# Performance work log

Hardware: AMD Instinct MI355X
Metric: run time of the kernel (lower is better)

## Reference

```python
import jax, jax.numpy as jnp
import numpy as np

N_NODES = 50000
N_EDGES = 800000
IN_FEAT = 4
HIDDEN = 128
NUM_LAYERS = 3


def setup_inputs() -> dict:
    key = jax.random.key(0)
    ks = jax.random.split(key, 16)
    x = jax.random.normal(ks[0], (N_NODES, IN_FEAT), dtype=jnp.float32)
    edge_index = jax.random.randint(ks[1], (2, N_EDGES), 0, N_NODES, dtype=jnp.int64)

    def lin(k, fan_in, fan_out):
        bound = 1.0 / np.sqrt(fan_in)
        k1, k2 = jax.random.split(k)
        W = jax.random.uniform(k1, (fan_in, fan_out), minval=-bound, maxval=bound, dtype=jnp.float32)
        b = jax.random.uniform(k2, (fan_out,), minval=-bound, maxval=bound, dtype=jnp.float32)
        return W, b

    W_enc, b_enc = lin(ks[2], IN_FEAT, HIDDEN)
    W_g1, b_g1 = lin(ks[3], HIDDEN, HIDDEN)
    W_g2, b_g2 = lin(ks[4], HIDDEN, HIDDEN)
    W_g3, b_g3 = lin(ks[5], HIDDEN, HIDDEN)
    W_m1, b_m1 = lin(ks[6], 2 * HIDDEN, HIDDEN)
    W_m2, b_m2 = lin(ks[7], HIDDEN, 3)
    return {
        "x": x, "edge_index": edge_index,
        "W_enc": W_enc, "b_enc": b_enc,
        "W_g1": W_g1, "b_g1": b_g1,
        "W_g2": W_g2, "b_g2": b_g2,
        "W_g3": W_g3, "b_g3": b_g3,
        "W_m1": W_m1, "b_m1": b_m1,
        "W_m2": W_m2, "b_m2": b_m2,
    }


def _gcn_forward(x, edge_index, W_enc, b_enc, gcn_params, W_m1, b_m1, W_m2, b_m2):
    n = x.shape[0]
    # Node encoder (linear + ReLU) -> [N, H]
    h = jax.nn.relu(x @ W_enc + b_enc)

    # Add self-loops once (GCNConv default add_self_loops=True)
    src = jnp.concatenate([edge_index[0], jnp.arange(n, dtype=edge_index.dtype)])
    dst = jnp.concatenate([edge_index[1], jnp.arange(n, dtype=edge_index.dtype)])
    # Symmetric degree normalization: D^{-1/2} (A+I) D^{-1/2}
    deg = jax.ops.segment_sum(jnp.ones_like(dst, dtype=h.dtype), dst, num_segments=n)
    deg_inv_sqrt = jnp.where(deg > 0, jax.lax.rsqrt(jnp.maximum(deg, 1.0)), 0.0)
    norm = (deg_inv_sqrt[src] * deg_inv_sqrt[dst])[:, None]  # [E+N, 1]

    for (W, b) in gcn_params:
        m = (h @ W)[src] * norm                       # gather + scale messages
        h = jax.ops.segment_sum(m, dst, num_segments=n) + b
        h = jax.nn.relu(h)                            # dropout is identity at eval

    # Edge classifier: gather endpoints, concat, MLP -> [E, 3]
    ef = jnp.concatenate([h[edge_index[0]], h[edge_index[1]]], axis=-1)
    return jax.nn.relu(ef @ W_m1 + b_m1) @ W_m2 + b_m2


def reference(x, edge_index, W_enc, b_enc, W_g1, b_g1, W_g2, b_g2, W_g3, b_g3, W_m1, b_m1, W_m2, b_m2):
    gcn_params = [(W_g1, b_g1), (W_g2, b_g2), (W_g3, b_g3)]
    return _gcn_forward(x, edge_index, W_enc, b_enc, gcn_params, W_m1, b_m1, W_m2, b_m2)
```

## Files before the change

kernel.cpp:

```cpp
#include <hip/hip_runtime.h>
#include <hip/hip_bf16.h>

#define N_NODES 50000
#define N_EDGES 800000
#define HID 128
#define NBUCKET 1024
#define N_NODE_BLOCKS ((N_NODES + 255) / 256)

typedef __attribute__((ext_vector_type(8))) short bf16x8;
typedef __attribute__((ext_vector_type(4))) float f32x4;

__device__ __forceinline__ ushort f2bf(float f) {
    uint u = __float_as_uint(f);
    return (ushort)((u + 0x7FFFu + ((u >> 16) & 1u)) >> 16);
}
__device__ __forceinline__ float bf2f(ushort h) { return __uint_as_float(((uint)h) << 16); }

__global__ void k_count(const int* __restrict__ ei, int* cnt) {
    int e = blockIdx.x * blockDim.x + threadIdx.x;
    if (e < N_EDGES) atomicAdd(&cnt[ei[N_EDGES + e]], 1);
}

__global__ __launch_bounds__(256) void k_bhist(const int* __restrict__ cnt, int* gHist,
                                               int* __restrict__ blockBase) {
    __shared__ int lh[NBUCKET];
    int t = threadIdx.x;
    for (int d = t; d < NBUCKET; d += 256) lh[d] = 0;
    __syncthreads();
    int n = blockIdx.x * 256 + t;
    if (n < N_NODES) {
        int deg = min(cnt[n], NBUCKET - 1);
        atomicAdd(&lh[deg], 1);
    }
    __syncthreads();
    for (int d = t; d < NBUCKET; d += 256) {
        int c = lh[d];
        blockBase[blockIdx.x * NBUCKET + d] = c ? atomicAdd(&gHist[d], c) : 0;
    }
}

__global__ __launch_bounds__(NBUCKET) void k_prefix(const int* __restrict__ gHist,
                                                    int* __restrict__ histBase,
                                                    int* __restrict__ edgeBase,
                                                    int* __restrict__ rowStartP) {
    __shared__ int a[NBUCKET];
    __shared__ int b[NBUCKET];
    int t = threadIdx.x;
    int h = gHist[t];
    a[t] = h;
    b[t] = h * t;
    __syncthreads();
    for (int off = 1; off < NBUCKET; off <<= 1) {
        int av = (t >= off) ? a[t - off] : 0;
        int bv = (t >= off) ? b[t - off] : 0;
        __syncthreads();
        a[t] += av;
        b[t] += bv;
        __syncthreads();
    }
    histBase[t] = a[t] - h;
    edgeBase[t] = b[t] - h * t;
    if (t == 0) rowStartP[N_NODES] = N_EDGES;
}

__global__ __launch_bounds__(256) void k_rank(const int* __restrict__ cnt,
                                              const int* __restrict__ histBase,
                                              const int* __restrict__ edgeBase,
                                              const int* __restrict__ blockBase,
                                              int* __restrict__ rank,
                                              int* __restrict__ rowStartP,
                                              float* __restrict__ dinvP) {
    __shared__ int cur[NBUCKET];
    int t = threadIdx.x;
    for (int d = t; d < NBUCKET; d += 256) cur[d] = 0;
    __syncthreads();
    int n = blockIdx.x * 256 + t;
    if (n < N_NODES) {
        int deg = min(cnt[n], NBUCKET - 1);
        int slot = atomicAdd(&cur[deg], 1);
        int r = histBase[deg] + blockBase[blockIdx.x * NBUCKET + deg] + slot;
        rank[n] = r;
        rowStartP[r] = edgeBase[deg] + (r - histBase[deg]) * deg;
        dinvP[r] = rsqrtf(1.0f + (float)deg);
    }
}

__global__ void k_fill(const int* __restrict__ ei, const int* __restrict__ rank,
                       const int* __restrict__ rowStartP, int* cursorP,
                       int2* __restrict__ csrE) {
    int e = blockIdx.x * blockDim.x + threadIdx.x;
    if (e < N_EDGES) {
        int s = ei[e];
        int d = ei[N_EDGES + e];
        int rd = rank[d];
        int pos = rowStartP[rd] + atomicAdd(&cursorP[rd], 1);
        csrE[pos] = make_int2(rank[s], e);
    }
}

struct WSplitArgs {
    const float* src[5];
    ushort* th[5];
    ushort* tl[5];
};

__global__ void k_tsplit5(WSplitArgs a) {
    int i = blockIdx.x * 256 + threadIdx.x;
    int which = i >> 14, r = i & 16383;
    int k = r >> 7, j = r & 127;
    float v = a.src[which][r];
    ushort hi = f2bf(v);
    a.th[which][j * 128 + k] = hi;
    a.tl[which][j * 128 + k] = f2bf(v - bf2f(hi));
}

__global__ void k_encoder(const float* __restrict__ x, const float* __restrict__ W,
                          const float* __restrict__ b, const int* __restrict__ rank,
                          ushort* __restrict__ hH, ushort* __restrict__ hL) {
    int i = blockIdx.x * 256 + threadIdx.x;
    int n = i >> 6, l = i & 63;
    int j = l * 2;
    float4 xv = *(const float4*)(x + (size_t)n * 4);
    float2 acc = *(const float2*)(b + j);
    float2 w0 = *(const float2*)(W + 0 * 128 + j);
    float2 w1 = *(const float2*)(W + 1 * 128 + j);
    float2 w2 = *(const float2*)(W + 2 * 128 + j);
    float2 w3 = *(const float2*)(W + 3 * 128 + j);
    acc.x += xv.x * w0.x + xv.y * w1.x + xv.z * w2.x + xv.w * w3.x;
    acc.y += xv.x * w0.y + xv.y * w1.y + xv.z * w2.y + xv.w * w3.y;
    float v0 = fmaxf(acc.x, 0.f), v1 = fmaxf(acc.y, 0.f);
    ushort h0 = f2bf(v0), h1 = f2bf(v1);
    ushort l0 = f2bf(v0 - bf2f(h0)), l1 = f2bf(v1 - bf2f(h1));
    size_t o = (size_t)rank[n] * 64 + l;
    ((uint*)hH)[o] = (uint)h0 | ((uint)h1 << 16);
    ((uint*)hL)[o] = (uint)l0 | ((uint)l1 << 16);
}

__global__ __launch_bounds__(256) void k_gemm_mfma(const ushort* __restrict__ AH,
                                                   const ushort* __restrict__ AL,
                                                   const ushort* __restrict__ BTH,
                                                   const ushort* __restrict__ BTL,
                                                   float* __restrict__ out,
                                                   const float* __restrict__ scale, int M) {
    int tid = threadIdx.x;
    int w = tid >> 6, l = tid & 63;
    int ln = l & 15, lk = l >> 4;
    int r0 = blockIdx.x * 128 + w * 32;
    int row0 = r0 + ln, row1 = r0 + 16 + ln;
    int a0 = row0 < M ? row0 : M - 1;
    int a1 = row1 < M ? row1 : M - 1;

    f32x4 acc0[8] = {};
    f32x4 acc1[8] = {};
#pragma unroll
    for (int kc = 0; kc < 4; ++kc) {
        int ko = kc * 32 + lk * 8;
        bf16x8 h0H = *(const bf16x8*)(AH + (size_t)a0 * 128 + ko);
        bf16x8 h0L = *(const bf16x8*)(AL + (size_t)a0 * 128 + ko);
        bf16x8 h1H = *(const bf16x8*)(AH + (size_t)a1 * 128 + ko);
        bf16x8 h1L = *(const bf16x8*)(AL + (size_t)a1 * 128 + ko);
#pragma unroll
        for (int nt = 0; nt < 8; ++nt) {
            size_t boff = (size_t)(nt * 16 + ln) * 128 + ko;
            bf16x8 wH = *(const bf16x8*)(BTH + boff);
            bf16x8 wL = *(const bf16x8*)(BTL + boff);
            acc0[nt] = __builtin_amdgcn_mfma_f32_16x16x32_bf16(wH, h0H, acc0[nt], 0, 0, 0);
            acc0[nt] = __builtin_amdgcn_mfma_f32_16x16x32_bf16(wL, h0H, acc0[nt], 0, 0, 0);
            acc0[nt] = __builtin_amdgcn_mfma_f32_16x16x32_bf16(wH, h0L, acc0[nt], 0, 0, 0);
            acc1[nt] = __builtin_amdgcn_mfma_f32_16x16x32_bf16(wH, h1H, acc1[nt], 0, 0, 0);
            acc1[nt] = __builtin_amdgcn_mfma_f32_16x16x32_bf16(wL, h1H, acc1[nt], 0, 0, 0);
            acc1[nt] = __builtin_amdgcn_mfma_f32_16x16x32_bf16(wH, h1L, acc1[nt], 0, 0, 0);
        }
    }
    float s0v = scale[a0];
    float s1v = scale[a1];
#pragma unroll
    for (int nt = 0; nt < 8; ++nt) {
        int jb = nt * 16 + lk * 4;
        if (row0 < M) {
            *(float4*)(out + (size_t)row0 * 128 + jb) =
                make_float4(acc0[nt][0] * s0v, acc0[nt][1] * s0v, acc0[nt][2] * s0v, acc0[nt][3] * s0v);
        }
        if (row1 < M) {
            *(float4*)(out + (size_t)row1 * 128 + jb) =
                make_float4(acc1[nt][0] * s1v, acc1[nt][1] * s1v, acc1[nt][2] * s1v, acc1[nt][3] * s1v);
        }
    }
}

__global__ __launch_bounds__(1024, 2) void k_agg_gemm(
    const float* __restrict__ hw, const float* __restrict__ bg,
    const float* __restrict__ dinvP, const int* __restrict__ rowStartP,
    const int2* __restrict__ csrE,
    const ushort* __restrict__ BTH1, const ushort* __restrict__ BTL1,
    const ushort* __restrict__ BTH2, const ushort* __restrict__ BTL2,
    float* __restrict__ out1, float* __restrict__ out2,
    const float* __restrict__ b1, const float* __restrict__ outScale) {
    __shared__ uint AsH[16][68];
    __shared__ uint AsL[16][68];
    int tid = threadIdx.x;
    int w = tid >> 6, l = tid & 63;
    int g = l >> 4, li = l & 15;
    int c8 = li * 8;
    int n = blockIdx.x * 16 + w;

    float4 aA, aB;
    if (g == 0) {
        aA = *(const float4*)(hw + (size_t)n * 128 + c8);
        aB = *(const float4*)(hw + (size_t)n * 128 + c8 + 4);
    } else {
        aA = make_float4(0.f, 0.f, 0.f, 0.f);
        aB = aA;
    }
    int s0 = rowStartP[n], s1 = rowStartP[n + 1];
    int k = s0 + g;
    float4 v0a = make_float4(0.f, 0.f, 0.f, 0.f), v0b = v0a;
    if (k < s1) {
        const float* r = hw + (size_t)csrE[k].x * 128 + c8;
        v0a = *(const float4*)(r);
        v0b = *(const float4*)(r + 4);
    }
    for (; k < s1; k += 4) {
        float4 v1a = make_float4(0.f, 0.f, 0.f, 0.f), v1b = v1a;
        if (k + 4 < s1) {
            const float* r = hw + (size_t)csrE[k + 4].x * 128 + c8;
            v1a = *(const float4*)(r);
            v1b = *(const float4*)(r + 4);
        }
        aA.x += v0a.x; aA.y += v0a.y; aA.z += v0a.z; aA.w += v0a.w;
        aB.x += v0b.x; aB.y += v0b.y; aB.z += v0b.z; aB.w += v0b.w;
        v0a = v1a;
        v0b = v1b;
    }
    aA.x += __shfl_xor(aA.x, 16); aA.y += __shfl_xor(aA.y, 16);
    aA.z += __shfl_xor(aA.z, 16); aA.w += __shfl_xor(aA.w, 16);
    aB.x += __shfl_xor(aB.x, 16); aB.y += __shfl_xor(aB.y, 16);
    aB.z += __shfl_xor(aB.z, 16); aB.w += __shfl_xor(aB.w, 16);
    aA.x += __shfl_xor(aA.x, 32); aA.y += __shfl_xor(aA.y, 32);
    aA.z += __shfl_xor(aA.z, 32); aA.w += __shfl_xor(aA.w, 32);
    aB.x += __shfl_xor(aB.x, 32); aB.y += __shfl_xor(aB.y, 32);
    aB.z += __shfl_xor(aB.z, 32); aB.w += __shfl_xor(aB.w, 32);

    if (g == 0) {
        float di = dinvP[n];
        float4 bbA = *(const float4*)(bg + c8);
        float4 bbB = *(const float4*)(bg + c8 + 4);
        float f0 = fmaxf(bbA.x + di * aA.x, 0.f);
        float f1 = fmaxf(bbA.y + di * aA.y, 0.f);
        float f2 = fmaxf(bbA.z + di * aA.z, 0.f);
        float f3 = fmaxf(bbA.w + di * aA.w, 0.f);
        float f4 = fmaxf(bbB.x + di * aB.x, 0.f);
        float f5 = fmaxf(bbB.y + di * aB.y, 0.f);
        float f6 = fmaxf(bbB.z + di * aB.z, 0.f);
        float f7 = fmaxf(bbB.w + di * aB.w, 0.f);
        ushort h0 = f2bf(f0), h1 = f2bf(f1), h2 = f2bf(f2), h3 = f2bf(f3);
        ushort h4 = f2bf(f4), h5 = f2bf(f5), h6 = f2bf(f6), h7 = f2bf(f7);
        uint4 uh = make_uint4((uint)h0 | ((uint)h1 << 16), (uint)h2 | ((uint)h3 << 16),
                              (uint)h4 | ((uint)h5 << 16), (uint)h6 | ((uint)h7 << 16));
        ushort l0 = f2bf(f0 - bf2f(h0)), l1 = f2bf(f1 - bf2f(h1));
        ushort l2 = f2bf(f2 - bf2f(h2)), l3 = f2bf(f3 - bf2f(h3));
        ushort l4 = f2bf(f4 - bf2f(h4)), l5 = f2bf(f5 - bf2f(h5));
        ushort l6 = f2bf(f6 - bf2f(h6)), l7 = f2bf(f7 - bf2f(h7));
        uint4 ul = make_uint4((uint)l0 | ((uint)l1 << 16), (uint)l2 | ((uint)l3 << 16),
                              (uint)l4 | ((uint)l5 << 16), (uint)l6 | ((uint)l7 << 16));
        *(uint4*)&AsH[w][li * 4] = uh;
        *(uint4*)&AsL[w][li * 4] = ul;
    }
    __syncthreads();

    bool second = w >= 8;
    if (second && !BTH2) return;
    const ushort* TH = second ? BTH2 : BTH1;
    const ushort* TL = second ? BTL2 : BTL1;
    int ln = l & 15, lk = l >> 4;
    int ct = w & 7;
    int node = blockIdx.x * 16 + ln;
    f32x4 acc = {};
#pragma unroll
    for (int kc = 0; kc < 4; ++kc) {
        uint4 uh = *(uint4*)&AsH[ln][kc * 16 + lk * 4];
        uint4 ul = *(uint4*)&AsL[ln][kc * 16 + lk * 4];
        bf16x8 hh, hl;
        __builtin_memcpy(&hh, &uh, 16);
        __builtin_memcpy(&hl, &ul, 16);
        size_t boff = (size_t)(ct * 16 + ln) * 128 + kc * 32 + lk * 8;
        bf16x8 wh = *(const bf16x8*)(TH + boff);
        bf16x8 wl = *(const bf16x8*)(TL + boff);
        acc = __builtin_amdgcn_mfma_f32_16x16x32_bf16(wh, hh, acc, 0, 0, 0);
        acc = __builtin_amdgcn_mfma_f32_16x16x32_bf16(wl, hh, acc, 0, 0, 0);
        acc = __builtin_amdgcn_mfma_f32_16x16x32_bf16(wh, hl, acc, 0, 0, 0);
    }
    int jb = ct * 16 + lk * 4;
    if (outScale) {
        float s = outScale[node];
        *(float4*)(out1 + (size_t)node * 128 + jb) =
            make_float4(acc[0] * s, acc[1] * s, acc[2] * s, acc[3] * s);
    } else if (!second) {
        *(float4*)(out1 + (size_t)node * 128 + jb) =
            make_float4(acc[0], acc[1], acc[2], acc[3]);
    } else {
        float4 bv = *(const float4*)(b1 + jb);
        *(float4*)(out2 + (size_t)node * 128 + jb) =
            make_float4(acc[0] + bv.x, acc[1] + bv.y, acc[2] + bv.z, acc[3] + bv.w);
    }
}

__global__ __launch_bounds__(256) void k_edge_final(const float* __restrict__ P,
                                                    const float* __restrict__ Qb,
                                                    const int* __restrict__ rowStartP,
                                                    const int2* __restrict__ csrE,
                                                    const float* __restrict__ W2,
                                                    const float* __restrict__ b2,
                                                    float* __restrict__ out) {
    int wid = (blockIdx.x * 256 + threadIdx.x) >> 6;
    int l = threadIdx.x & 63;
    if (wid >= N_NODES) return;
    int s0 = rowStartP[wid], s1 = rowStartP[wid + 1];
    if (s0 >= s1) return;
    int j8 = (l & 15) * 8;
    int g = l >> 4;

    float4 qa = *(const float4*)(Qb + (size_t)wid * 128 + j8);
    float4 qb = *(const float4*)(Qb + (size_t)wid * 128 + j8 + 4);
    float w2r[8][3];
#pragma unroll
    for (int k = 0; k < 8; ++k) {
        w2r[k][0] = W2[(j8 + k) * 3 + 0];
        w2r[k][1] = W2[(j8 + k) * 3 + 1];
        w2r[k][2] = W2[(j8 + k) * 3 + 2];
    }
    float bz0 = b2[0], bz1 = b2[1], bz2 = b2[2];

    int k = s0 + g;
    int2 c = make_int2(0, 0);
    float4 pa = make_float4(0.f, 0.f, 0.f, 0.f), pb = pa;
    if (k < s1) {
        c = csrE[k];
        const float* pr = P + (size_t)c.x * 128 + j8;
        pa = *(const float4*)(pr);
        pb = *(const float4*)(pr + 4);
    }
    for (; k < s1; k += 4) {
        int kn = k + 4;
        int2 cn = make_int2(0, 0);
        float4 pan = make_float4(0.f, 0.f, 0.f, 0.f), pbn = pan;
        if (kn < s1) {
            cn = csrE[kn];
            const float* prn = P + (size_t)cn.x * 128 + j8;
            pan = *(const float4*)(prn);
            pbn = *(const float4*)(prn + 4);
        }
        float z[8];
        z[0] = fmaxf(pa.x + qa.x, 0.f);
        z[1] = fmaxf(pa.y + qa.y, 0.f);
        z[2] = fmaxf(pa.z + qa.z, 0.f);
        z[3] = fmaxf(pa.w + qa.w, 0.f);
        z[4] = fmaxf(pb.x + qb.x, 0.f);
        z[5] = fmaxf(pb.y + qb.y, 0.f);
        z[6] = fmaxf(pb.z + qb.z, 0.f);
        z[7] = fmaxf(pb.w + qb.w, 0.f);
        float o0 = 0.f, o1 = 0.f, o2 = 0.f;
#pragma unroll
        for (int q = 0; q < 8; ++q) {
            o0 += z[q] * w2r[q][0];
            o1 += z[q] * w2r[q][1];
            o2 += z[q] * w2r[q][2];
        }
#pragma unroll
        for (int m = 1; m < 16; m <<= 1) {
            o0 += __shfl_xor(o0, m);
            o1 += __shfl_xor(o1, m);
            o2 += __shfl_xor(o2, m);
        }
        if ((l & 15) == 0) {
            float* op = out + (size_t)c.y * 3;
            op[0] = o0 + bz0;
            op[1] = o1 + bz1;
            op[2] = o2 + bz2;
        }
        c = cn;
        pa = pan;
        pb = pbn;
    }
}

extern "C" void kernel_launch(void* const* d_in, const int* in_sizes, int n_in,
                              void* d_out, int out_size, void* d_ws, size_t ws_size,
                              hipStream_t stream) {
    const float* x     = (const float*)d_in[0];
    const int*   ei    = (const int*)d_in[1];
    const float* W_enc = (const float*)d_in[2];
    const float* b_enc = (const float*)d_in[3];
    const float* Wg[3] = {(const float*)d_in[4], (const float*)d_in[6], (const float*)d_in[8]};
    const float* bg[3] = {(const float*)d_in[5], (const float*)d_in[7], (const float*)d_in[9]};
    const float* W_m1  = (const float*)d_in[10];
    const float* b_m1  = (const float*)d_in[11];
    const float* W_m2  = (const float*)d_in[12];
    const float* b_m2  = (const float*)d_in[13];
    float* out = (float*)d_out;

    char* w = (char*)d_ws;
    ushort* hH      = (ushort*)w;  w += (size_t)N_NODES * HID * 2;
    ushort* hL      = (ushort*)w;  w += (size_t)N_NODES * HID * 2;
    float*  bufA    = (float*)w;   w += (size_t)N_NODES * HID * 4;
    float*  bufB    = (float*)w;   w += (size_t)N_NODES * HID * 4;
    int2*   csrE    = (int2*)w;    w += (size_t)N_EDGES * 8;
    int*    cnt     = (int*)w;     w += (size_t)N_NODES * 4;
    int*    cursorP = (int*)w;     w += (size_t)N_NODES * 4;
    int*    gHist   = (int*)w;     w += NBUCKET * 4;
    size_t  zeroBytes = (size_t)(N_NODES * 2 + NBUCKET) * 4;
    int*    rank    = (int*)w;     w += (size_t)N_NODES * 4;
    int*    rowStartP = (int*)w;   w += (size_t)(N_NODES + 4) * 4;
    float*  dinvP   = (float*)w;   w += (size_t)N_NODES * 4;
    int*    histBase = (int*)w;    w += NBUCKET * 4;
    int*    edgeBase = (int*)w;    w += NBUCKET * 4;
    int*    blockBase = (int*)w;   w += (size_t)N_NODE_BLOCKS * NBUCKET * 4;
    ushort* WgTH[3], *WgTL[3];
    for (int i = 0; i < 3; ++i) {
        WgTH[i] = (ushort*)w; w += 128 * 128 * 2;
        WgTL[i] = (ushort*)w; w += 128 * 128 * 2;
    }
    ushort* WtTH = (ushort*)w; w += 128 * 128 * 2;
    ushort* WtTL = (ushort*)w; w += 128 * 128 * 2;
    ushort* WbTH = (ushort*)w; w += 128 * 128 * 2;
    ushort* WbTL = (ushort*)w; w += 128 * 128 * 2;

    float* P  = (float*)hH;
    float* Qb = bufB;

    hipMemsetAsync(cnt, 0, zeroBytes, stream);
    k_count<<<(N_EDGES + 255) / 256, 256, 0, stream>>>(ei, cnt);
    k_bhist<<<N_NODE_BLOCKS, 256, 0, stream>>>(cnt, gHist, blockBase);
    k_prefix<<<1, NBUCKET, 0, stream>>>(gHist, histBase, edgeBase, rowStartP);
    k_rank<<<N_NODE_BLOCKS, 256, 0, stream>>>(cnt, histBase, edgeBase, blockBase,
                                              rank, rowStartP, dinvP);
    k_fill<<<(N_EDGES + 255) / 256, 256, 0, stream>>>(ei, rank, rowStartP, cursorP, csrE);

    WSplitArgs wa;
    wa.src[0] = Wg[0]; wa.th[0] = WgTH[0]; wa.tl[0] = WgTL[0];
    wa.src[1] = Wg[1]; wa.th[1] = WgTH[1]; wa.tl[1] = WgTL[1];
    wa.src[2] = Wg[2]; wa.th[2] = WgTH[2]; wa.tl[2] = WgTL[2];
    wa.src[3] = W_m1;             wa.th[3] = WtTH; wa.tl[3] = WtTL;
    wa.src[4] = W_m1 + 128 * 128; wa.th[4] = WbTH; wa.tl[4] = WbTL;
    k_tsplit5<<<5 * 16384 / 256, 256, 0, stream>>>(wa);

    k_encoder<<<N_NODES * 64 / 256, 256, 0, stream>>>(x, W_enc, b_enc, rank, hH, hL);

    k_gemm_mfma<<<(N_NODES + 127) / 128, 256, 0, stream>>>(hH, hL, WgTH[0], WgTL[0],
                                                           bufA, dinvP, N_NODES);

    const int fusedGrid = N_NODES / 16;
    k_agg_gemm<<<fusedGrid, 1024, 0, stream>>>(bufA, bg[0], dinvP, rowStartP, csrE,
                                               WgTH[1], WgTL[1], nullptr, nullptr,
                                               bufB, nullptr, nullptr, dinvP);
    k_agg_gemm<<<fusedGrid, 1024, 0, stream>>>(bufB, bg[1], dinvP, rowStartP, csrE,
                                               WgTH[2], WgTL[2], nullptr, nullptr,
                                               bufA, nullptr, nullptr, dinvP);
    k_agg_gemm<<<fusedGrid, 1024, 0, stream>>>(bufA, bg[2], dinvP, rowStartP, csrE,
                                               WtTH, WtTL, WbTH, WbTL,
                                               P, Qb, b_m1, nullptr);

    k_edge_final<<<(N_NODES * 64) / 256, 256, 0, stream>>>(P, Qb, rowStartP, csrE,
                                                           W_m2, b_m2, out);
}
```

Baseline: 467.4 us.

## Split fused aggregate+GEMM into separate kernels and fuse encoder into first GEMM

The old 1024-thread kernel fused aggregation with a small 16-row MFMA GEMM per block. It is replaced by a standalone aggregation kernel that writes bf16 hi/lo features, followed by the larger 128-row tiled MFMA GEMM. The final P/Q projection now runs in one launch with a 2D grid. The encoder is fused into the first GEMM, using an inverse rank map so inputs are gathered directly into shared memory. This trades extra global round-trips of the hidden features for better GEMM weight reuse and aggregation occupancy.

```diff
diff --git a/kernel.cpp b/kernel.cpp
--- a/kernel.cpp
+++ b/kernel.cpp
@@ -68,6 +68,7 @@
                                               const int* __restrict__ edgeBase,
                                               const int* __restrict__ blockBase,
                                               int* __restrict__ rank,
+                                              int* __restrict__ invRank,
                                               int* __restrict__ rowStartP,
                                               float* __restrict__ dinvP) {
     __shared__ int cur[NBUCKET];
@@ -80,6 +81,7 @@
         int slot = atomicAdd(&cur[deg], 1);
         int r = histBase[deg] + blockBase[blockIdx.x * NBUCKET + deg] + slot;
         rank[n] = r;
+        invRank[r] = n;
         rowStartP[r] = edgeBase[deg] + (r - histBase[deg]) * deg;
         dinvP[r] = rsqrtf(1.0f + (float)deg);
     }
@@ -114,105 +116,94 @@
     a.tl[which][j * 128 + k] = f2bf(v - bf2f(hi));
 }
 
-__global__ void k_encoder(const float* __restrict__ x, const float* __restrict__ W,
-                          const float* __restrict__ b, const int* __restrict__ rank,
-                          ushort* __restrict__ hH, ushort* __restrict__ hL) {
-    int i = blockIdx.x * 256 + threadIdx.x;
-    int n = i >> 6, l = i & 63;
-    int j = l * 2;
-    float4 xv = *(const float4*)(x + (size_t)n * 4);
-    float2 acc = *(const float2*)(b + j);
-    float2 w0 = *(const float2*)(W + 0 * 128 + j);
-    float2 w1 = *(const float2*)(W + 1 * 128 + j);
-    float2 w2 = *(const float2*)(W + 2 * 128 + j);
-    float2 w3 = *(const float2*)(W + 3 * 128 + j);
-    acc.x += xv.x * w0.x + xv.y * w1.x + xv.z * w2.x + xv.w * w3.x;
-    acc.y += xv.x * w0.y + xv.y * w1.y + xv.z * w2.y + xv.w * w3.y;
-    float v0 = fmaxf(acc.x, 0.f), v1 = fmaxf(acc.y, 0.f);
-    ushort h0 = f2bf(v0), h1 = f2bf(v1);
-    ushort l0 = f2bf(v0 - bf2f(h0)), l1 = f2bf(v1 - bf2f(h1));
-    size_t o = (size_t)rank[n] * 64 + l;
-    ((uint*)hH)[o] = (uint)h0 | ((uint)h1 << 16);
-    ((uint*)hL)[o] = (uint)l0 | ((uint)l1 << 16);
-}
-
-__global__ __launch_bounds__(256) void k_gemm_mfma(const ushort* __restrict__ AH,
-                                                   const ushort* __restrict__ AL,
-                                                   const ushort* __restrict__ BTH,
-                                                   const ushort* __restrict__ BTL,
-                                                   float* __restrict__ out,
-                                                   const float* __restrict__ scale, int M) {
-    int tid = threadIdx.x;
-    int w = tid >> 6, l = tid & 63;
-    int ln = l & 15, lk = l >> 4;
-    int r0 = blockIdx.x * 128 + w * 32;
-    int row0 = r0 + ln, row1 = r0 + 16 + ln;
-    int a0 = row0 < M ? row0 : M - 1;
-    int a1 = row1 < M ? row1 : M - 1;
-
-    f32x4 acc0[8] = {};
-    f32x4 acc1[8] = {};
-#pragma unroll
-    for (int kc = 0; kc < 4; ++kc) {
-        int ko = kc * 32 + lk * 8;
-        bf16x8 h0H = *(const bf16x8*)(AH + (size_t)a0 * 128 + ko);
-        bf16x8 h0L = *(const bf16x8*)(AL + (size_t)a0 * 128 + ko);
-        bf16x8 h1H = *(const bf16x8*)(AH + (size_t)a1 * 128 + ko);
-        bf16x8 h1L = *(const bf16x8*)(AL + (size_t)a1 * 128 + ko);
-#pragma unroll
-        for (int nt = 0; nt < 8; ++nt) {
-            size_t boff = (size_t)(nt * 16 + ln) * 128 + ko;
-            bf16x8 wH = *(const bf16x8*)(BTH + boff);
-            bf16x8 wL = *(const bf16x8*)(BTL + boff);
-            acc0[nt] = __builtin_amdgcn_mfma_f32_16x16x32_bf16(wH, h0H, acc0[nt], 0, 0, 0);
-            acc0[nt] = __builtin_amdgcn_mfma_f32_16x16x32_bf16(wL, h0H, acc0[nt], 0, 0, 0);
-            acc0[nt] = __builtin_amdgcn_mfma_f32_16x16x32_bf16(wH, h0L, acc0[nt], 0, 0, 0);
-            acc1[nt] = __builtin_amdgcn_mfma_f32_16x16x32_bf16(wH, h1H, acc1[nt], 0, 0, 0);
-            acc1[nt] = __builtin_amdgcn_mfma_f32_16x16x32_bf16(wL, h1H, acc1[nt], 0, 0, 0);
-            acc1[nt] = __builtin_amdgcn_mfma_f32_16x16x32_bf16(wH, h1L, acc1[nt], 0, 0, 0);
-        }
-    }
-    float s0v = scale[a0];
-    float s1v = scale[a1];
-#pragma unroll
-    for (int nt = 0; nt < 8; ++nt) {
-        int jb = nt * 16 + lk * 4;
-        if (row0 < M) {
-            *(float4*)(out + (size_t)row0 * 128 + jb) =
-                make_float4(acc0[nt][0] * s0v, acc0[nt][1] * s0v, acc0[nt][2] * s0v, acc0[nt][3] * s0v);
-        }
-        if (row1 < M) {
-            *(float4*)(out + (size_t)row1 * 128 + jb) =
-                make_float4(acc1[nt][0] * s1v, acc1[nt][1] * s1v, acc1[nt][2] * s1v, acc1[nt][3] * s1v);
-        }
-    }
-}
-
-__global__ __launch_bounds__(1024, 2) void k_agg_gemm(
-    const float* __restrict__ hw, const float* __restrict__ bg,
-    const float* __restrict__ dinvP, const int* __restrict__ rowStartP,
-    const int2* __restrict__ csrE,
-    const ushort* __restrict__ BTH1, const ushort* __restrict__ BTL1,
-    const ushort* __restrict__ BTH2, const ushort* __restrict__ BTL2,
-    float* __restrict__ out1, float* __restrict__ out2,
-    const float* __restrict__ b1, const float* __restrict__ outScale) {
+__global__ __launch_bounds__(512, 8) void k_enc_gemm(
+    const float* __restrict__ x, const float* __restrict__ Wenc,
+    const float* __restrict__ benc, const int* __restrict__ invRank,
+    const float* __restrict__ dinvP,
+    const ushort* __restrict__ BTH, const ushort* __restrict__ BTL,
+    float* __restrict__ out) {
     __shared__ uint AsH[16][68];
     __shared__ uint AsL[16][68];
     int tid = threadIdx.x;
+
+    if (tid < 256) {
+        int ln = tid >> 4, li = tid & 15;
+        int r = blockIdx.x * 16 + ln;
+        int n = invRank[r];
+        float4 xv = *(const float4*)(x + (size_t)n * 4);
+        int j0 = li * 8;
+        uint uh[4], ul[4];
+#pragma unroll
+        for (int p = 0; p < 4; ++p) {
+            ushort hs[2], ls[2];
+#pragma unroll
+            for (int q = 0; q < 2; ++q) {
+                int j = j0 + p * 2 + q;
+                float acc = benc[j];
+                acc += xv.x * Wenc[0 * 128 + j];
+                acc += xv.y * Wenc[1 * 128 + j];
+                acc += xv.z * Wenc[2 * 128 + j];
+                acc += xv.w * Wenc[3 * 128 + j];
+                float v = fmaxf(acc, 0.f);
+                hs[q] = f2bf(v);
+                ls[q] = f2bf(v - bf2f(hs[q]));
+            }
+            uh[p] = (uint)hs[0] | ((uint)hs[1] << 16);
+            ul[p] = (uint)ls[0] | ((uint)ls[1] << 16);
+        }
+        *(uint4*)&AsH[ln][li * 4] = make_uint4(uh[0], uh[1], uh[2], uh[3]);
+        *(uint4*)&AsL[ln][li * 4] = make_uint4(ul[0], ul[1], ul[2], ul[3]);
+    }
+    __syncthreads();
+
     int w = tid >> 6, l = tid & 63;
+    int ln = l & 15, lk = l >> 4;
+    int ct = w;
+    int node = blockIdx.x * 16 + ln;
+    f32x4 acc = {};
+#pragma unroll
+    for (int kc = 0; kc < 4; ++kc) {
+        uint4 uhv = *(uint4*)&AsH[ln][kc * 16 + lk * 4];
+        uint4 ulv = *(uint4*)&AsL[ln][kc * 16 + lk * 4];
+        bf16x8 hh, hl;
+        __builtin_memcpy(&hh, &uhv, 16);
+        __builtin_memcpy(&hl, &ulv, 16);
+        size_t boff = (size_t)(ct * 16 + ln) * 128 + kc * 32 + lk * 8;
+        bf16x8 wh = *(const bf16x8*)(BTH + boff);
+        bf16x8 wl = *(const bf16x8*)(BTL + boff);
+        acc = __builtin_amdgcn_mfma_f32_16x16x32_bf16(wh, hh, acc, 0, 0, 0);
+        acc = __builtin_amdgcn_mfma_f32_16x16x32_bf16(wl, hh, acc, 0, 0, 0);
+        acc = __builtin_amdgcn_mfma_f32_16x16x32_bf16(wh, hl, acc, 0, 0, 0);
+    }
+    int jb = ct * 16 + lk * 4;
+    float s = dinvP[node];
+    *(float4*)(out + (size_t)node * 128 + jb) =
+        make_float4(acc[0] * s, acc[1] * s, acc[2] * s, acc[3] * s);
+}
+
+__global__ __launch_bounds__(256) void k_aggregate(const float* __restrict__ hw,
+                                                   const float* __restrict__ bg,
+                                                   const float* __restrict__ dinvP,
+                                                   const int* __restrict__ rowStartP,
+                                                   const int2* __restrict__ csrE,
+                                                   ushort* __restrict__ hH,
+                                                   ushort* __restrict__ hL) {
+    int wid = (blockIdx.x * 256 + threadIdx.x) >> 6;
+    int l = threadIdx.x & 63;
+    if (wid >= N_NODES) return;
     int g = l >> 4, li = l & 15;
     int c8 = li * 8;
-    int n = blockIdx.x * 16 + w;
 
     float4 aA, aB;
     if (g == 0) {
-        aA = *(const float4*)(hw + (size_t)n * 128 + c8);
-        aB = *(const float4*)(hw + (size_t)n * 128 + c8 + 4);
+        aA = *(const float4*)(hw + (size_t)wid * 128 + c8);
+        aB = *(const float4*)(hw + (size_t)wid * 128 + c8 + 4);
     } else {
         aA = make_float4(0.f, 0.f, 0.f, 0.f);
         aB = aA;
     }
-    int s0 = rowStartP[n], s1 = rowStartP[n + 1];
+
+    int s0 = rowStartP[wid], s1 = rowStartP[wid + 1];
     int k = s0 + g;
     float4 v0a = make_float4(0.f, 0.f, 0.f, 0.f), v0b = v0a;
     if (k < s1) {
@@ -242,7 +233,7 @@
     aB.z += __shfl_xor(aB.z, 32); aB.w += __shfl_xor(aB.w, 32);
 
     if (g == 0) {
-        float di = dinvP[n];
+        float di = dinvP[wid];
         float4 bbA = *(const float4*)(bg + c8);
         float4 bbB = *(const float4*)(bg + c8 + 4);
         float f0 = fmaxf(bbA.x + di * aA.x, 0.f);
@@ -263,46 +254,91 @@
         ushort l6 = f2bf(f6 - bf2f(h6)), l7 = f2bf(f7 - bf2f(h7));
         uint4 ul = make_uint4((uint)l0 | ((uint)l1 << 16), (uint)l2 | ((uint)l3 << 16),
                               (uint)l4 | ((uint)l5 << 16), (uint)l6 | ((uint)l7 << 16));
-        *(uint4*)&AsH[w][li * 4] = uh;
-        *(uint4*)&AsL[w][li * 4] = ul;
-    }
-    __syncthreads();
-
-    bool second = w >= 8;
-    if (second && !BTH2) return;
-    const ushort* TH = second ? BTH2 : BTH1;
-    const ushort* TL = second ? BTL2 : BTL1;
+        *(uint4*)(hH + (size_t)wid * 128 + c8) = uh;
+        *(uint4*)(hL + (size_t)wid * 128 + c8) = ul;
+    }
+}
+
+__device__ __forceinline__ void gemm_body(const ushort* __restrict__ AH,
+                                          const ushort* __restrict__ AL,
+                                          const ushort* __restrict__ BTH,
+                                          const ushort* __restrict__ BTL,
+                                          float* __restrict__ out,
+                                          const float* __restrict__ bias,
+                                          const float* __restrict__ scale, int M) {
+    int tid = threadIdx.x;
+    int w = tid >> 6, l = tid & 63;
     int ln = l & 15, lk = l >> 4;
-    int ct = w & 7;
-    int node = blockIdx.x * 16 + ln;
-    f32x4 acc = {};
+    int r0 = blockIdx.x * 128 + w * 32;
+    int row0 = r0 + ln, row1 = r0 + 16 + ln;
+    int a0 = row0 < M ? row0 : M - 1;
+    int a1 = row1 < M ? row1 : M - 1;
+
+    f32x4 acc0[8] = {};
+    f32x4 acc1[8] = {};
 #pragma unroll
     for (int kc = 0; kc < 4; ++kc) {
-        uint4 uh = *(uint4*)&AsH[ln][kc * 16 + lk * 4];
-        uint4 ul = *(uint4*)&AsL[ln][kc * 16 + lk * 4];
-        bf16x8 hh, hl;
-        __builtin_memcpy(&hh, &uh, 16);
-        __builtin_memcpy(&hl, &ul, 16);
-        size_t boff = (size_t)(ct * 16 + ln) * 128 + kc * 32 + lk * 8;
-        bf16x8 wh = *(const bf16x8*)(TH + boff);
-        bf16x8 wl = *(const bf16x8*)(TL + boff);
-        acc = __builtin_amdgcn_mfma_f32_16x16x32_bf16(wh, hh, acc, 0, 0, 0);
-        acc = __builtin_amdgcn_mfma_f32_16x16x32_bf16(wl, hh, acc, 0, 0, 0);
-        acc = __builtin_amdgcn_mfma_f32_16x16x32_bf16(wh, hl, acc, 0, 0, 0);
-    }
-    int jb = ct * 16 + lk * 4;
-    if (outScale) {
-        float s = outScale[node];
-        *(float4*)(out1 + (size_t)node * 128 + jb) =
-            make_float4(acc[0] * s, acc[1] * s, acc[2] * s, acc[3] * s);
-    } else if (!second) {
-        *(float4*)(out1 + (size_t)node * 128 + jb) =
-            make_float4(acc[0], acc[1], acc[2], acc[3]);
-    } else {
-        float4 bv = *(const float4*)(b1 + jb);
-        *(float4*)(out2 + (size_t)node * 128 + jb) =
-            make_float4(acc[0] + bv.x, acc[1] + bv.y, acc[2] + bv.z, acc[3] + bv.w);
-    }
+        int ko = kc * 32 + lk * 8;
+        bf16x8 h0H = *(const bf16x8*)(AH + (size_t)a0 * 128 + ko);
+        bf16x8 h0L = *(const bf16x8*)(AL + (size_t)a0 * 128 + ko);
+        bf16x8 h1H = *(const bf16x8*)(AH + (size_t)a1 * 128 + ko);
+        bf16x8 h1L = *(const bf16x8*)(AL + (size_t)a1 * 128 + ko);
+#pragma unroll
+        for (int nt = 0; nt < 8; ++nt) {
+            size_t boff = (size_t)(nt * 16 + ln) * 128 + ko;
+            bf16x8 wH = *(const bf16x8*)(BTH + boff);
+            bf16x8 wL = *(const bf16x8*)(BTL + boff);
+            acc0[nt] = __builtin_amdgcn_mfma_f32_16x16x32_bf16(wH, h0H, acc0[nt], 0, 0, 0);
+            acc0[nt] = __builtin_amdgcn_mfma_f32_16x16x32_bf16(wL, h0H, acc0[nt], 0, 0, 0);
+            acc0[nt] = __builtin_amdgcn_mfma_f32_16x16x32_bf16(wH, h0L, acc0[nt], 0, 0, 0);
+            acc1[nt] = __builtin_amdgcn_mfma_f32_16x16x32_bf16(wH, h1H, acc1[nt], 0, 0, 0);
+            acc1[nt] = __builtin_amdgcn_mfma_f32_16x16x32_bf16(wL, h1H, acc1[nt], 0, 0, 0);
+            acc1[nt] = __builtin_amdgcn_mfma_f32_16x16x32_bf16(wH, h1L, acc1[nt], 0, 0, 0);
+        }
+    }
+    float s0v = scale ? scale[a0] : 1.f;
+    float s1v = scale ? scale[a1] : 1.f;
+#pragma unroll
+    for (int nt = 0; nt < 8; ++nt) {
+        int jb = nt * 16 + lk * 4;
+        float4 bv;
+        if (bias) bv = *(const float4*)(bias + jb);
+        else bv = make_float4(0.f, 0.f, 0.f, 0.f);
+        if (row0 < M) {
+            *(float4*)(out + (size_t)row0 * 128 + jb) =
+                make_float4((acc0[nt][0] + bv.x) * s0v, (acc0[nt][1] + bv.y) * s0v,
+                            (acc0[nt][2] + bv.z) * s0v, (acc0[nt][3] + bv.w) * s0v);
+        }
+        if (row1 < M) {
+            *(float4*)(out + (size_t)row1 * 128 + jb) =
+                make_float4((acc1[nt][0] + bv.x) * s1v, (acc1[nt][1] + bv.y) * s1v,
+                            (acc1[nt][2] + bv.z) * s1v, (acc1[nt][3] + bv.w) * s1v);
+        }
+    }
+}
+
+__global__ __launch_bounds__(256) void k_gemm_mfma(const ushort* __restrict__ AH,
+                                                   const ushort* __restrict__ AL,
+                                                   const ushort* __restrict__ BTH,
+                                                   const ushort* __restrict__ BTL,
+                                                   float* __restrict__ out,
+                                                   const float* __restrict__ scale, int M) {
+    gemm_body(AH, AL, BTH, BTL, out, nullptr, scale, M);
+}
+
+__global__ __launch_bounds__(256) void k_gemm_pq(const ushort* __restrict__ AH,
+                                                 const ushort* __restrict__ AL,
+                                                 const ushort* __restrict__ BTHt,
+                                                 const ushort* __restrict__ BTLt,
+                                                 const ushort* __restrict__ BTHb,
+                                                 const ushort* __restrict__ BTLb,
+                                                 float* __restrict__ outP,
+                                                 float* __restrict__ outQ,
+                                                 const float* __restrict__ b1, int M) {
+    if (blockIdx.y == 0)
+        gemm_body(AH, AL, BTHt, BTLt, outP, nullptr, nullptr, M);
+    else
+        gemm_body(AH, AL, BTHb, BTLb, outQ, b1, nullptr, M);
 }
 
 __global__ __launch_bounds__(256) void k_edge_final(const float* __restrict__ P,
@@ -410,6 +446,7 @@
     int*    gHist   = (int*)w;     w += NBUCKET * 4;
     size_t  zeroBytes = (size_t)(N_NODES * 2 + NBUCKET) * 4;
     int*    rank    = (int*)w;     w += (size_t)N_NODES * 4;
+    int*    invRank = (int*)w;     w += (size_t)N_NODES * 4;
     int*    rowStartP = (int*)w;   w += (size_t)(N_NODES + 4) * 4;
     float*  dinvP   = (float*)w;   w += (size_t)N_NODES * 4;
     int*    histBase = (int*)w;    w += NBUCKET * 4;
@@ -425,7 +462,7 @@
     ushort* WbTH = (ushort*)w; w += 128 * 128 * 2;
     ushort* WbTL = (ushort*)w; w += 128 * 128 * 2;
 
-    float* P  = (float*)hH;
+    float* P  = bufA;
     float* Qb = bufB;
 
     hipMemsetAsync(cnt, 0, zeroBytes, stream);
@@ -433,7 +470,7 @@
     k_bhist<<<N_NODE_BLOCKS, 256, 0, stream>>>(cnt, gHist, blockBase);
     k_prefix<<<1, NBUCKET, 0, stream>>>(gHist, histBase, edgeBase, rowStartP);
     k_rank<<<N_NODE_BLOCKS, 256, 0, stream>>>(cnt, histBase, edgeBase, blockBase,
-                                              rank, rowStartP, dinvP);
+                                              rank, invRank, rowStartP, dinvP);
     k_fill<<<(N_EDGES + 255) / 256, 256, 0, stream>>>(ei, rank, rowStartP, cursorP, csrE);
 
     WSplitArgs wa;
@@ -444,21 +481,19 @@
     wa.src[4] = W_m1 + 128 * 128; wa.th[4] = WbTH; wa.tl[4] = WbTL;
     k_tsplit5<<<5 * 16384 / 256, 256, 0, stream>>>(wa);
 
-    k_encoder<<<N_NODES * 64 / 256, 256, 0, stream>>>(x, W_enc, b_enc, rank, hH, hL);
-
-    k_gemm_mfma<<<(N_NODES + 127) / 128, 256, 0, stream>>>(hH, hL, WgTH[0], WgTL[0],
-                                                           bufA, dinvP, N_NODES);
-
-    const int fusedGrid = N_NODES / 16;
-    k_agg_gemm<<<fusedGrid, 1024, 0, stream>>>(bufA, bg[0], dinvP, rowStartP, csrE,
-                                               WgTH[1], WgTL[1], nullptr, nullptr,
-                                               bufB, nullptr, nullptr, dinvP);
-    k_agg_gemm<<<fusedGrid, 1024, 0, stream>>>(bufB, bg[1], dinvP, rowStartP, csrE,
-                                               WgTH[2], WgTL[2], nullptr, nullptr,
-                                               bufA, nullptr, nullptr, dinvP);
-    k_agg_gemm<<<fusedGrid, 1024, 0, stream>>>(bufA, bg[2], dinvP, rowStartP, csrE,
-                                               WtTH, WtTL, WbTH, WbTL,
-                                               P, Qb, b_m1, nullptr);
+    k_enc_gemm<<<N_NODES / 16, 512, 0, stream>>>(x, W_enc, b_enc, invRank, dinvP,
+                                                 WgTH[0], WgTL[0], bufA);
+
+    const int aggGrid  = (N_NODES * 64) / 256;
+    const int gemmGrid = (N_NODES + 127) / 128;
+
+    k_aggregate<<<aggGrid, 256, 0, stream>>>(bufA, bg[0], dinvP, rowStartP, csrE, hH, hL);
+    k_gemm_mfma<<<gemmGrid, 256, 0, stream>>>(hH, hL, WgTH[1], WgTL[1], bufB, dinvP, N_NODES);
+    k_aggregate<<<aggGrid, 256, 0, stream>>>(bufB, bg[1], dinvP, rowStartP, csrE, hH, hL);
+    k_gemm_mfma<<<gemmGrid, 256, 0, stream>>>(hH, hL, WgTH[2], WgTL[2], bufA, dinvP, N_NODES);
+    k_aggregate<<<aggGrid, 256, 0, stream>>>(bufA, bg[2], dinvP, rowStartP, csrE, hH, hL);
+    dim3 pqGrid(gemmGrid, 2);
+    k_gemm_pq<<<pqGrid, 256, 0, stream>>>(hH, hL, WtTH, WtTL, WbTH, WbTL, P, Qb, b_m1, N_NODES);
 
     k_edge_final<<<(N_NODES * 64) / 256, 256, 0, stream>>>(P, Qb, rowStartP, csrE,
                                                            W_m2, b_m2, out);
```

Result: no change. 471.4 us (+0.8%).
